# Optimization experiments

Measured on AMD Instinct MI355X. Metric: run time of the kernel, lower is better.

Reference implementation:

```python
import jax, jax.numpy as jnp
import numpy as np

N = 100000       # nodes
E = 1600000      # edges (before self-loops)
D = 128          # input feature dim
H = 128          # hidden width (both hidden GATConv layers)
OUT = 128        # out_channel
NEG_SLOPE = 0.2  # PyG GATConv default


def setup_inputs() -> dict:
    key = jax.random.key(0)
    ks = jax.random.split(key, 16)
    x = jax.random.normal(ks[0], (N, D), dtype=jnp.float32)
    edge_index = jax.random.randint(ks[1], (2, E), 0, N, dtype=jnp.int64)

    def layer_params(k, din, dout):
        k1, k2, k3 = jax.random.split(k, 3)
        W = jax.random.normal(k1, (din, dout), dtype=jnp.float32) * (1.0 / np.sqrt(din))
        a_src = jax.random.normal(k2, (dout,), dtype=jnp.float32) * 0.1
        a_dst = jax.random.normal(k3, (dout,), dtype=jnp.float32) * 0.1
        b = jnp.zeros((dout,), dtype=jnp.float32)
        return W, a_src, a_dst, b

    W0, as0, ad0, b0 = layer_params(ks[2], D, H)
    W1, as1, ad1, b1 = layer_params(ks[3], H, H)
    W2, as2, ad2, b2 = layer_params(ks[4], H, OUT)
    return {
        "x": x, "edge_index": edge_index,
        "W0": W0, "as0": as0, "ad0": ad0, "b0": b0,
        "W1": W1, "as1": as1, "ad1": ad1, "b1": b1,
        "W2": W2, "as2": as2, "ad2": ad2, "b2": b2,
    }


def _gat_conv(x, src, dst, W, a_src, a_dst, b):
    """PyG GATConv, heads=1: gather -> edge attention softmax (per dst) -> scatter-add."""
    h = x @ W                                  # [N, C]
    alpha_s = h @ a_src                        # [N] per-source scalar
    alpha_d = h @ a_dst                        # [N] per-dest scalar
    e = jax.nn.leaky_relu(alpha_s[src] + alpha_d[dst], NEG_SLOPE)  # [Etot]
    # numerically stable softmax over edges grouped by destination node
    m = jax.ops.segment_max(e, dst, num_segments=N)
    ex = jnp.exp(e - m[dst])
    denom = jax.ops.segment_sum(ex, dst, num_segments=N)
    w = ex / denom[dst]                        # [Etot] attention coeffs
    out = jax.ops.segment_sum(h[src] * w[:, None], dst, num_segments=N)
    return out + b


def reference(x, edge_index, W0, as0, ad0, b0, W1, as1, ad1, b1, W2, as2, ad2, b2):
    # GATConv adds self-loops by default; edge_index[0]=source j, [1]=target i
    loops = jnp.arange(N, dtype=edge_index.dtype)
    src = jnp.concatenate([edge_index[0], loops])
    dst = jnp.concatenate([edge_index[1], loops])

    h = jax.nn.relu(_gat_conv(x, src, dst, W0, as0, ad0, b0))
    h = jax.nn.relu(_gat_conv(h, src, dst, W1, as1, ad1, b1))
    return _gat_conv(h, src, dst, W2, as2, ad2, b2)
```

## Files before the change

kernel.cpp:

```cpp
#include <hip/hip_runtime.h>

#define NN 100000
#define EE 1600000
#define NB 391
#define CHUNK 2048

typedef __attribute__((ext_vector_type(8))) short bf16x8;
typedef __attribute__((ext_vector_type(4))) float f32x4;

union BV8 { bf16x8 v; uint4 u; };

static __device__ __forceinline__ unsigned short f2bf(float f) {
  unsigned u = __float_as_uint(f);
  u += 0x7fffu + ((u >> 16) & 1u);
  return (unsigned short)(u >> 16);
}
static __device__ __forceinline__ float bf2f(unsigned short s) {
  return __uint_as_float(((unsigned)s) << 16);
}
static __device__ __forceinline__ unsigned cvt_pk_bf16(float a, float b) {
  unsigned r;
  asm("v_cvt_pk_bf16_f32 %0, %1, %2" : "=v"(r) : "v"(a), "v"(b));
  return r;
}
static __device__ __forceinline__ float bflo(unsigned u) { return __uint_as_float(u << 16); }
static __device__ __forceinline__ float bfhi(unsigned u) { return __uint_as_float(u & 0xffff0000u); }


__global__ void zero_aux(int* __restrict__ bcnt, int* __restrict__ bfill) {
  int i = blockIdx.x * 256 + threadIdx.x;
  if (i < NB * 16) { bcnt[i] = 0; bfill[i] = 0; }
}

__launch_bounds__(256)
__global__ void bucket_hist(const int* __restrict__ dst, int* __restrict__ bcnt) {
  __shared__ int hist[NB];
  int tid = threadIdx.x;
  for (int i = tid; i < NB; i += 256) hist[i] = 0;
  __syncthreads();
  int e0 = blockIdx.x * CHUNK;
  int n = min(CHUNK, EE - e0);
  for (int i = tid; i < n; i += 256) atomicAdd(&hist[dst[e0 + i] >> 8], 1);
  __syncthreads();
  for (int i = tid; i < NB; i += 256) {
    int c = hist[i];
    if (c) atomicAdd(&bcnt[i * 16], c);
  }
}

__launch_bounds__(256)
__global__ void bucket_scan(const int* __restrict__ bcnt, int* __restrict__ bOffC,
                            int* __restrict__ offsets) {
  __shared__ int wpart[4];
  __shared__ int carryS;
  int tid = threadIdx.x, lane = tid & 63, w = tid >> 6;
  if (tid == 0) carryS = 0;
  __syncthreads();
  for (int base = 0; base < NB; base += 256) {
    int i = base + tid;
    int v = (i < NB) ? bcnt[i * 16] : 0;
    int x = v;
    #pragma unroll
    for (int d = 1; d < 64; d <<= 1) { int y = __shfl_up(x, d); if (lane >= d) x += y; }
    if (lane == 63) wpart[w] = x;
    __syncthreads();
    int wbase = 0;
    #pragma unroll
    for (int k = 0; k < 3; ++k) if (k < w) wbase += wpart[k];
    int tot = wpart[0] + wpart[1] + wpart[2] + wpart[3];
    int carry = carryS;
    if (i < NB) bOffC[i] = carry + wbase + x - v;
    __syncthreads();
    if (tid == 0) carryS = carry + tot;
    __syncthreads();
  }
  if (tid == 0) offsets[NN] = EE + NN;
}

__launch_bounds__(256)
__global__ void bucket_scatter(const int* __restrict__ ei, const int* __restrict__ bOffC,
                               int* __restrict__ bfill, long long* __restrict__ pairs) {
  __shared__ int hist[NB];
  __shared__ int lofs[NB];
  __shared__ int resv[NB];
  __shared__ long long stage[CHUNK];
  __shared__ int wpart[4];
  int tid = threadIdx.x, lane = tid & 63, w = tid >> 6;
  int e0 = blockIdx.x * CHUNK;
  int n = min(CHUNK, EE - e0);
  for (int i = tid; i < NB; i += 256) hist[i] = 0;
  __syncthreads();

  int s[8], d[8], lp[8], bk[8];
  #pragma unroll
  for (int q = 0; q < 8; ++q) {
    int i = q * 256 + tid;
    if (i < n) {
      s[q] = ei[e0 + i];
      d[q] = ei[EE + e0 + i];
      bk[q] = d[q] >> 8;
      lp[q] = atomicAdd(&hist[bk[q]], 1);
    }
  }
  __syncthreads();

  int carry = 0;
  for (int base = 0; base < NB; base += 256) {
    int i = base + tid;
    int v = (i < NB) ? hist[i] : 0;
    int x = v;
    #pragma unroll
    for (int dd = 1; dd < 64; dd <<= 1) { int y = __shfl_up(x, dd); if (lane >= dd) x += y; }
    if (lane == 63) wpart[w] = x;
    __syncthreads();
    int wbase = 0;
    #pragma unroll
    for (int k = 0; k < 3; ++k) if (k < w) wbase += wpart[k];
    int tot = wpart[0] + wpart[1] + wpart[2] + wpart[3];
    if (i < NB) lofs[i] = carry + wbase + x - v;
    __syncthreads();
    carry += tot;
  }

  #pragma unroll
  for (int q = 0; q < 8; ++q) {
    int i = q * 256 + tid;
    if (i < n) stage[lofs[bk[q]] + lp[q]] = ((long long)d[q] << 32) | (unsigned)s[q];
  }
  for (int b = tid; b < NB; b += 256) {
    int c = hist[b];
    resv[b] = c ? atomicAdd(&bfill[b * 16], c) : 0;
  }
  __syncthreads();
  for (int i = tid; i < n; i += 256) {
    long long pd = stage[i];
    int dd = (int)(pd >> 32);
    int b = dd >> 8;
    pairs[(size_t)bOffC[b] + resv[b] + (i - lofs[b])] = pd;
  }
}

__launch_bounds__(256)
__global__ void build_csr(const long long* __restrict__ pairs, const int* __restrict__ bOffC,
                          const int* __restrict__ bcnt, int* __restrict__ offsets,
                          int* __restrict__ srcs) {
  __shared__ int deg[256];
  __shared__ int intra[256];
  __shared__ int fil[256];
  __shared__ int wpart[4];
  int b = blockIdx.x, tid = threadIdx.x;
  int n0 = b << 8;
  int nodes = min(256, NN - n0);
  int ecnt = bcnt[b * 16];
  size_t pbase = (size_t)bOffC[b];
  int cbase = bOffC[b] + n0;
  deg[tid] = 0; fil[tid] = 0;
  __syncthreads();
  for (int i = tid; i < ecnt; i += 256) {
    int dd = (int)(pairs[pbase + i] >> 32);
    atomicAdd(&deg[dd - n0], 1);
  }
  __syncthreads();
  int v = (tid < nodes) ? deg[tid] + 1 : 0;
  int lane = tid & 63, w = tid >> 6;
  int x = v;
  #pragma unroll
  for (int dd = 1; dd < 64; dd <<= 1) { int y = __shfl_up(x, dd); if (lane >= dd) x += y; }
  if (lane == 63) wpart[w] = x;
  __syncthreads();
  int wbase = 0;
  #pragma unroll
  for (int k = 0; k < 3; ++k) if (k < w) wbase += wpart[k];
  int excl = wbase + x - v;
  if (tid < nodes) { intra[tid] = excl; offsets[n0 + tid] = cbase + excl; }
  __syncthreads();
  for (int i = tid; i < ecnt; i += 256) {
    long long pd = pairs[pbase + i];
    int dd = (int)(pd >> 32), ss = (int)pd;
    int ln = dd - n0;
    int p = atomicAdd(&fil[ln], 1);
    srcs[cbase + intra[ln] + p] = ss;
  }
  __syncthreads();
  if (tid < nodes) srcs[cbase + intra[tid] + deg[tid]] = n0 + tid;
}


__global__ void prep_w3(const float* __restrict__ Wa, const float* __restrict__ Wb,
                        const float* __restrict__ Wc, short* __restrict__ Whi,
                        short* __restrict__ Wlo) {
  int t = blockIdx.x * 256 + threadIdx.x;
  int L = t >> 11;
  int tt = t & 2047;
  const float* W = (L == 0) ? Wa : (L == 1) ? Wb : Wc;
  int lane = tt & 63, ct = (tt >> 6) & 7, kt = tt >> 9;
  int l4 = lane & 15, grp = lane >> 4;
  int c = ct * 16 + l4;
  int k0 = kt * 32 + grp * 8;
  bf16x8 hi, lo;
  #pragma unroll
  for (int i = 0; i < 8; ++i) {
    float w = W[(k0 + i) * 128 + c];
    unsigned short h = f2bf(w);
    hi[i] = (short)h;
    lo[i] = (short)f2bf(w - bf2f(h));
  }
  size_t off = (size_t)L * 131072 + ((size_t)(kt * 8 + ct) * 64 + lane) * 8;
  *(bf16x8*)&Whi[off] = hi;
  *(bf16x8*)&Wlo[off] = lo;
}


__launch_bounds__(256)
__global__ void transform_mfma(const float* __restrict__ x,
                               const short* __restrict__ Whi, const short* __restrict__ Wlo,
                               const float* __restrict__ a_src, const float* __restrict__ a_dst,
                               unsigned short* __restrict__ hb,
                               float* __restrict__ alphaS, float* __restrict__ alphaD) {
  __shared__ short WhiS[4096];
  __shared__ short WloS[4096];
  int tid = threadIdx.x;
  int lane = tid & 63, wid = tid >> 6;
  int l4 = lane & 15, grp = lane >> 4;
  int rbase = blockIdx.x * 128 + wid * 32;

  const float* xr[2];
  #pragma unroll
  for (int rt = 0; rt < 2; ++rt) {
    int R = rbase + rt * 16 + l4;
    xr[rt] = x + (size_t)(R < NN ? R : 0) * 128;
  }

  f32x4 acc[2][8];
  #pragma unroll
  for (int rt = 0; rt < 2; ++rt)
    #pragma unroll
    for (int ct = 0; ct < 8; ++ct) acc[rt][ct] = (f32x4)(0.f);

  for (int kt = 0; kt < 4; ++kt) {
    bf16x8 Ahi[2], Alo[2];
    #pragma unroll
    for (int rt = 0; rt < 2; ++rt) {
      const float* p = xr[rt] + kt * 32 + grp * 8;
      float4 v0 = *(const float4*)p;
      float4 v1 = *(const float4*)(p + 4);
      BV8 hi, lo;
      hi.u.x = cvt_pk_bf16(v0.x, v0.y);
      hi.u.y = cvt_pk_bf16(v0.z, v0.w);
      hi.u.z = cvt_pk_bf16(v1.x, v1.y);
      hi.u.w = cvt_pk_bf16(v1.z, v1.w);
      lo.u.x = cvt_pk_bf16(v0.x - bflo(hi.u.x), v0.y - bfhi(hi.u.x));
      lo.u.y = cvt_pk_bf16(v0.z - bflo(hi.u.y), v0.w - bfhi(hi.u.y));
      lo.u.z = cvt_pk_bf16(v1.x - bflo(hi.u.z), v1.y - bfhi(hi.u.z));
      lo.u.w = cvt_pk_bf16(v1.z - bflo(hi.u.w), v1.w - bfhi(hi.u.w));
      Ahi[rt] = hi.v;
      Alo[rt] = lo.v;
    }
    __syncthreads();
    {
      int base = kt * 4096 + tid * 16;
      *(bf16x8*)&WhiS[tid * 16]     = *(const bf16x8*)&Whi[base];
      *(bf16x8*)&WhiS[tid * 16 + 8] = *(const bf16x8*)&Whi[base + 8];
      *(bf16x8*)&WloS[tid * 16]     = *(const bf16x8*)&Wlo[base];
      *(bf16x8*)&WloS[tid * 16 + 8] = *(const bf16x8*)&Wlo[base + 8];
    }
    __syncthreads();
    #pragma unroll
    for (int ct = 0; ct < 8; ++ct) {
      bf16x8 bh = *(const bf16x8*)&WhiS[(ct * 64 + lane) * 8];
      bf16x8 bl = *(const bf16x8*)&WloS[(ct * 64 + lane) * 8];
      #pragma unroll
      for (int rt = 0; rt < 2; ++rt) {
        acc[rt][ct] = __builtin_amdgcn_mfma_f32_16x16x32_bf16(Ahi[rt], bh, acc[rt][ct], 0, 0, 0);
        acc[rt][ct] = __builtin_amdgcn_mfma_f32_16x16x32_bf16(Ahi[rt], bl, acc[rt][ct], 0, 0, 0);
        acc[rt][ct] = __builtin_amdgcn_mfma_f32_16x16x32_bf16(Alo[rt], bh, acc[rt][ct], 0, 0, 0);
      }
    }
  }

  float asv[8], adv[8];
  #pragma unroll
  for (int ct = 0; ct < 8; ++ct) { asv[ct] = a_src[ct * 16 + l4]; adv[ct] = a_dst[ct * 16 + l4]; }

  #pragma unroll
  for (int rt = 0; rt < 2; ++rt) {
    #pragma unroll
    for (int reg = 0; reg < 4; ++reg) {
      float ps = 0.f, pd = 0.f;
      #pragma unroll
      for (int ct = 0; ct < 8; ++ct) {
        ps = fmaf(acc[rt][ct][reg], asv[ct], ps);
        pd = fmaf(acc[rt][ct][reg], adv[ct], pd);
      }
      #pragma unroll
      for (int mdl = 1; mdl < 16; mdl <<= 1) {
        ps += __shfl_xor(ps, mdl);
        pd += __shfl_xor(pd, mdl);
      }
      int row = rbase + rt * 16 + grp * 4 + reg;
      if (l4 == 0 && row < NN) { alphaS[row] = ps; alphaD[row] = pd; }
    }
    #pragma unroll
    for (int reg = 0; reg < 4; ++reg) {
      int row = rbase + rt * 16 + grp * 4 + reg;
      if (row < NN) {
        #pragma unroll
        for (int ct = 0; ct < 8; ct += 2) {
          unsigned u = cvt_pk_bf16(acc[rt][ct][reg], acc[rt][ct + 1][reg]);
          hb[(size_t)row * 128 + ct * 16 + l4]       = (unsigned short)u;
          hb[(size_t)row * 128 + (ct + 1) * 16 + l4] = (unsigned short)(u >> 16);
        }
      }
    }
  }
}


template<bool RELU>
__launch_bounds__(256)
__global__ void agg_kernel(const unsigned short* __restrict__ hb,
                           const float* __restrict__ alphaS, const float* __restrict__ alphaD,
                           const int* __restrict__ offsets, const int* __restrict__ srcs,
                           const float* __restrict__ bias, float* __restrict__ out) {
  int lane = threadIdx.x & 63;
  int node = (blockIdx.x * 256 + threadIdx.x) >> 6;
  if (node >= NN) return;
  int beg = offsets[node], end = offsets[node + 1];
  float aD = alphaD[node];

  int l4 = lane & 15, grp = lane >> 4;
  float a[8];
  #pragma unroll
  for (int i = 0; i < 8; ++i) a[i] = 0.f;
  float ssum = 0.f;

  for (int j0 = beg; j0 < end; j0 += 64) {
    int j = j0 + lane;
    int cnt = min(64, end - j0);
    int s = 0; float t = 0.f;
    if (j < end) {
      int sv = srcs[j];
      float e = alphaS[sv] + aD;
      e = (e >= 0.f) ? e : 0.2f * e;
      t = __expf(e);
      s = sv;
    }
    ssum += t;
    for (int jj = 0; jj < cnt; jj += 16) {
      int eA = jj + grp;
      int eB = eA + 4, eC = eA + 8, eD = eA + 12;
      int svA = __shfl(s, eA); float tA = __shfl(t, eA);
      int svB = __shfl(s, eB); float tB = __shfl(t, eB);
      int svC = __shfl(s, eC); float tC = __shfl(t, eC);
      int svD = __shfl(s, eD); float tD = __shfl(t, eD);
      if (tA > 0.f) {
        uint4 h0 = *(const uint4*)&hb[(size_t)svA * 128 + l4 * 8];
        uint4 h1 = *(const uint4*)&hb[(size_t)svB * 128 + l4 * 8];
        a[0] = fmaf(tA, __uint_as_float(h0.x << 16),         a[0]);
        a[1] = fmaf(tA, __uint_as_float(h0.x & 0xffff0000u), a[1]);
        a[2] = fmaf(tA, __uint_as_float(h0.y << 16),         a[2]);
        a[3] = fmaf(tA, __uint_as_float(h0.y & 0xffff0000u), a[3]);
        a[4] = fmaf(tA, __uint_as_float(h0.z << 16),         a[4]);
        a[5] = fmaf(tA, __uint_as_float(h0.z & 0xffff0000u), a[5]);
        a[6] = fmaf(tA, __uint_as_float(h0.w << 16),         a[6]);
        a[7] = fmaf(tA, __uint_as_float(h0.w & 0xffff0000u), a[7]);
        a[0] = fmaf(tB, __uint_as_float(h1.x << 16),         a[0]);
        a[1] = fmaf(tB, __uint_as_float(h1.x & 0xffff0000u), a[1]);
        a[2] = fmaf(tB, __uint_as_float(h1.y << 16),         a[2]);
        a[3] = fmaf(tB, __uint_as_float(h1.y & 0xffff0000u), a[3]);
        a[4] = fmaf(tB, __uint_as_float(h1.z << 16),         a[4]);
        a[5] = fmaf(tB, __uint_as_float(h1.z & 0xffff0000u), a[5]);
        a[6] = fmaf(tB, __uint_as_float(h1.w << 16),         a[6]);
        a[7] = fmaf(tB, __uint_as_float(h1.w & 0xffff0000u), a[7]);
      }
      if (tC > 0.f) {
        uint4 h2 = *(const uint4*)&hb[(size_t)svC * 128 + l4 * 8];
        uint4 h3 = *(const uint4*)&hb[(size_t)svD * 128 + l4 * 8];
        a[0] = fmaf(tC, __uint_as_float(h2.x << 16),         a[0]);
        a[1] = fmaf(tC, __uint_as_float(h2.x & 0xffff0000u), a[1]);
        a[2] = fmaf(tC, __uint_as_float(h2.y << 16),         a[2]);
        a[3] = fmaf(tC, __uint_as_float(h2.y & 0xffff0000u), a[3]);
        a[4] = fmaf(tC, __uint_as_float(h2.z << 16),         a[4]);
        a[5] = fmaf(tC, __uint_as_float(h2.z & 0xffff0000u), a[5]);
        a[6] = fmaf(tC, __uint_as_float(h2.w << 16),         a[6]);
        a[7] = fmaf(tC, __uint_as_float(h2.w & 0xffff0000u), a[7]);
        a[0] = fmaf(tD, __uint_as_float(h3.x << 16),         a[0]);
        a[1] = fmaf(tD, __uint_as_float(h3.x & 0xffff0000u), a[1]);
        a[2] = fmaf(tD, __uint_as_float(h3.y << 16),         a[2]);
        a[3] = fmaf(tD, __uint_as_float(h3.y & 0xffff0000u), a[3]);
        a[4] = fmaf(tD, __uint_as_float(h3.z << 16),         a[4]);
        a[5] = fmaf(tD, __uint_as_float(h3.z & 0xffff0000u), a[5]);
        a[6] = fmaf(tD, __uint_as_float(h3.w << 16),         a[6]);
        a[7] = fmaf(tD, __uint_as_float(h3.w & 0xffff0000u), a[7]);
      }
    }
  }
  #pragma unroll
  for (int d2 = 1; d2 < 64; d2 <<= 1) ssum += __shfl_xor(ssum, d2);
  float inv = 1.f / ssum;

  #pragma unroll
  for (int i = 0; i < 8; ++i) {
    a[i] += __shfl_xor(a[i], 16);
    a[i] += __shfl_xor(a[i], 32);
  }
  if (grp == 0) {
    float4 b0 = *(const float4*)&bias[l4 * 8];
    float4 b1 = *(const float4*)&bias[l4 * 8 + 4];
    float4 o0 = {fmaf(a[0], inv, b0.x), fmaf(a[1], inv, b0.y),
                 fmaf(a[2], inv, b0.z), fmaf(a[3], inv, b0.w)};
    float4 o1 = {fmaf(a[4], inv, b1.x), fmaf(a[5], inv, b1.y),
                 fmaf(a[6], inv, b1.z), fmaf(a[7], inv, b1.w)};
    if (RELU) {
      o0.x = fmaxf(o0.x, 0.f); o0.y = fmaxf(o0.y, 0.f);
      o0.z = fmaxf(o0.z, 0.f); o0.w = fmaxf(o0.w, 0.f);
      o1.x = fmaxf(o1.x, 0.f); o1.y = fmaxf(o1.y, 0.f);
      o1.z = fmaxf(o1.z, 0.f); o1.w = fmaxf(o1.w, 0.f);
    }
    *(float4*)&out[(size_t)node * 128 + l4 * 8]     = o0;
    *(float4*)&out[(size_t)node * 128 + l4 * 8 + 4] = o1;
  }
}


extern "C" void kernel_launch(void* const* d_in, const int* in_sizes, int n_in,
                              void* d_out, int out_size, void* d_ws, size_t ws_size,
                              hipStream_t stream) {
  const float* x   = (const float*)d_in[0];
  const int*   ei  = (const int*)d_in[1];
  const float* W0  = (const float*)d_in[2];
  const float* as0 = (const float*)d_in[3];
  const float* ad0 = (const float*)d_in[4];
  const float* b0  = (const float*)d_in[5];
  const float* W1  = (const float*)d_in[6];
  const float* as1 = (const float*)d_in[7];
  const float* ad1 = (const float*)d_in[8];
  const float* b1  = (const float*)d_in[9];
  const float* W2  = (const float*)d_in[10];
  const float* as2 = (const float*)d_in[11];
  const float* ad2 = (const float*)d_in[12];
  const float* b2  = (const float*)d_in[13];
  float* out = (float*)d_out;

  long long* pairs = (long long*)d_ws;
  short* Whi = (short*)(pairs + EE);
  short* Wlo = Whi + 3 * 131072;
  unsigned short* hb = (unsigned short*)(Wlo + 3 * 131072);
  float* alphaS = (float*)(hb + (size_t)NN * 128);
  float* alphaD = alphaS + NN;
  int*   offsets = (int*)(alphaD + NN);
  int*   srcs    = offsets + NN + 1;
  int*   bcnt    = srcs + EE + NN;
  int*   bfill   = bcnt + NB * 16;
  int*   bOffC   = bfill + NB * 16;

  const int cgrid = (EE + CHUNK - 1) / CHUNK;

  prep_w3<<<24, 256, 0, stream>>>(W0, W1, W2, Whi, Wlo);
  zero_aux<<<(NB * 16 + 255) / 256, 256, 0, stream>>>(bcnt, bfill);
  bucket_hist<<<cgrid, 256, 0, stream>>>(ei + EE, bcnt);
  bucket_scan<<<1, 256, 0, stream>>>(bcnt, bOffC, offsets);
  bucket_scatter<<<cgrid, 256, 0, stream>>>(ei, bOffC, bfill, pairs);
  build_csr<<<NB, 256, 0, stream>>>(pairs, bOffC, bcnt, offsets, srcs);

  const int tgrid = (NN + 127) / 128;
  const int agrid = (NN + 3) / 4;

  transform_mfma<<<tgrid, 256, 0, stream>>>(x, Whi, Wlo, as0, ad0, hb, alphaS, alphaD);
  agg_kernel<true><<<agrid, 256, 0, stream>>>(hb, alphaS, alphaD, offsets, srcs, b0, out);

  transform_mfma<<<tgrid, 256, 0, stream>>>(out, Whi + 131072, Wlo + 131072, as1, ad1, hb, alphaS, alphaD);
  agg_kernel<true><<<agrid, 256, 0, stream>>>(hb, alphaS, alphaD, offsets, srcs, b1, out);

  transform_mfma<<<tgrid, 256, 0, stream>>>(out, Whi + 262144, Wlo + 262144, as2, ad2, hb, alphaS, alphaD);
  agg_kernel<false><<<agrid, 256, 0, stream>>>(hb, alphaS, alphaD, offsets, srcs, b2, out);
}
```

Baseline: 358.3 us.

## Fold attention vectors into GEMM tile and pack CSR pairs to 32 bits

Precomputes W·a_src and W·a_dst per layer and appends them as a ninth MFMA column tile, so alpha scores come straight out of the matrix multiply instead of per-row FMA and shuffle reductions. It also packs edge pairs as an 8-bit local destination plus a 24-bit source, which halves the bytes written by bucket_scatter and read by build_csr. In exchange, each transform does about 12% more MFMA work, and the alpha values are computed in a different rounding order.

```diff
diff --git a/kernel.cpp b/kernel.cpp
--- a/kernel.cpp
+++ b/kernel.cpp
@@ -4,6 +4,7 @@
 #define EE 1600000
 #define NB 391
 #define CHUNK 2048
+#define LFRAG 18432
 
 typedef __attribute__((ext_vector_type(8))) short bf16x8;
 typedef __attribute__((ext_vector_type(4))) float f32x4;
@@ -79,11 +80,12 @@
 
 __launch_bounds__(256)
 __global__ void bucket_scatter(const int* __restrict__ ei, const int* __restrict__ bOffC,
-                               int* __restrict__ bfill, long long* __restrict__ pairs) {
+                               int* __restrict__ bfill, unsigned* __restrict__ pairs) {
   __shared__ int hist[NB];
   __shared__ int lofs[NB];
   __shared__ int resv[NB];
-  __shared__ long long stage[CHUNK];
+  __shared__ unsigned stage[CHUNK];
+  __shared__ unsigned short stageB[CHUNK];
   __shared__ int wpart[4];
   int tid = threadIdx.x, lane = tid & 63, w = tid >> 6;
   int e0 = blockIdx.x * CHUNK;
@@ -125,7 +127,11 @@
   #pragma unroll
   for (int q = 0; q < 8; ++q) {
     int i = q * 256 + tid;
-    if (i < n) stage[lofs[bk[q]] + lp[q]] = ((long long)d[q] << 32) | (unsigned)s[q];
+    if (i < n) {
+      int p = lofs[bk[q]] + lp[q];
+      stage[p]  = ((unsigned)(d[q] & 255) << 24) | (unsigned)s[q];
+      stageB[p] = (unsigned short)bk[q];
+    }
   }
   for (int b = tid; b < NB; b += 256) {
     int c = hist[b];
@@ -133,15 +139,13 @@
   }
   __syncthreads();
   for (int i = tid; i < n; i += 256) {
-    long long pd = stage[i];
-    int dd = (int)(pd >> 32);
-    int b = dd >> 8;
-    pairs[(size_t)bOffC[b] + resv[b] + (i - lofs[b])] = pd;
-  }
-}
-
-__launch_bounds__(256)
-__global__ void build_csr(const long long* __restrict__ pairs, const int* __restrict__ bOffC,
+    int b = stageB[i];
+    pairs[(size_t)bOffC[b] + resv[b] + (i - lofs[b])] = stage[i];
+  }
+}
+
+__launch_bounds__(256)
+__global__ void build_csr(const unsigned* __restrict__ pairs, const int* __restrict__ bOffC,
                           const int* __restrict__ bcnt, int* __restrict__ offsets,
                           int* __restrict__ srcs) {
   __shared__ int deg[256];
@@ -157,8 +161,8 @@
   deg[tid] = 0; fil[tid] = 0;
   __syncthreads();
   for (int i = tid; i < ecnt; i += 256) {
-    int dd = (int)(pairs[pbase + i] >> 32);
-    atomicAdd(&deg[dd - n0], 1);
+    int ln = (int)(pairs[pbase + i] >> 24);
+    atomicAdd(&deg[ln], 1);
   }
   __syncthreads();
   int v = (tid < nodes) ? deg[tid] + 1 : 0;
@@ -175,9 +179,8 @@
   if (tid < nodes) { intra[tid] = excl; offsets[n0 + tid] = cbase + excl; }
   __syncthreads();
   for (int i = tid; i < ecnt; i += 256) {
-    long long pd = pairs[pbase + i];
-    int dd = (int)(pd >> 32), ss = (int)pd;
-    int ln = dd - n0;
+    unsigned pd = pairs[pbase + i];
+    int ln = (int)(pd >> 24), ss = (int)(pd & 0xFFFFFFu);
     int p = atomicAdd(&fil[ln], 1);
     srcs[cbase + intra[ln] + p] = ss;
   }
@@ -186,26 +189,56 @@
 }
 
 
+__global__ void prep_wavec(const float* __restrict__ Wa, const float* __restrict__ Wb,
+                           const float* __restrict__ Wc,
+                           const float* __restrict__ s0, const float* __restrict__ d0,
+                           const float* __restrict__ s1, const float* __restrict__ d1,
+                           const float* __restrict__ s2, const float* __restrict__ d2,
+                           float* __restrict__ was, float* __restrict__ wad) {
+  int t = blockIdx.x * 256 + threadIdx.x;
+  if (t >= 384) return;
+  int L = t >> 7, k = t & 127;
+  const float* W  = (L == 0) ? Wa : (L == 1) ? Wb : Wc;
+  const float* as = (L == 0) ? s0 : (L == 1) ? s1 : s2;
+  const float* ad = (L == 0) ? d0 : (L == 1) ? d1 : d2;
+  float accs = 0.f, accd = 0.f;
+  for (int c = 0; c < 128; c += 4) {
+    float4 w = *(const float4*)&W[k * 128 + c];
+    float4 a = *(const float4*)&as[c];
+    float4 b = *(const float4*)&ad[c];
+    accs += w.x * a.x + w.y * a.y + w.z * a.z + w.w * a.w;
+    accd += w.x * b.x + w.y * b.y + w.z * b.z + w.w * b.w;
+  }
+  was[t] = accs;
+  wad[t] = accd;
+}
+
 __global__ void prep_w3(const float* __restrict__ Wa, const float* __restrict__ Wb,
-                        const float* __restrict__ Wc, short* __restrict__ Whi,
+                        const float* __restrict__ Wc, const float* __restrict__ was,
+                        const float* __restrict__ wad, short* __restrict__ Whi,
                         short* __restrict__ Wlo) {
   int t = blockIdx.x * 256 + threadIdx.x;
-  int L = t >> 11;
-  int tt = t & 2047;
+  if (t >= 6912) return;
+  int L = t / 2304, tt = t % 2304;
+  int kt = tt / 576, rem = tt % 576;
+  int ct = rem >> 6, lane = rem & 63;
   const float* W = (L == 0) ? Wa : (L == 1) ? Wb : Wc;
-  int lane = tt & 63, ct = (tt >> 6) & 7, kt = tt >> 9;
   int l4 = lane & 15, grp = lane >> 4;
-  int c = ct * 16 + l4;
   int k0 = kt * 32 + grp * 8;
   bf16x8 hi, lo;
   #pragma unroll
   for (int i = 0; i < 8; ++i) {
-    float w = W[(k0 + i) * 128 + c];
+    float w;
+    if (ct < 8) {
+      w = W[(k0 + i) * 128 + ct * 16 + l4];
+    } else {
+      w = (l4 == 0) ? was[L * 128 + k0 + i] : (l4 == 1) ? wad[L * 128 + k0 + i] : 0.f;
+    }
     unsigned short h = f2bf(w);
     hi[i] = (short)h;
     lo[i] = (short)f2bf(w - bf2f(h));
   }
-  size_t off = (size_t)L * 131072 + ((size_t)(kt * 8 + ct) * 64 + lane) * 8;
+  size_t off = (size_t)L * LFRAG + ((size_t)(kt * 9 + ct) * 64 + lane) * 8;
   *(bf16x8*)&Whi[off] = hi;
   *(bf16x8*)&Wlo[off] = lo;
 }
@@ -214,11 +247,10 @@
 __launch_bounds__(256)
 __global__ void transform_mfma(const float* __restrict__ x,
                                const short* __restrict__ Whi, const short* __restrict__ Wlo,
-                               const float* __restrict__ a_src, const float* __restrict__ a_dst,
                                unsigned short* __restrict__ hb,
                                float* __restrict__ alphaS, float* __restrict__ alphaD) {
-  __shared__ short WhiS[4096];
-  __shared__ short WloS[4096];
+  __shared__ short WhiS[4608];
+  __shared__ short WloS[4608];
   int tid = threadIdx.x;
   int lane = tid & 63, wid = tid >> 6;
   int l4 = lane & 15, grp = lane >> 4;
@@ -231,11 +263,11 @@
     xr[rt] = x + (size_t)(R < NN ? R : 0) * 128;
   }
 
-  f32x4 acc[2][8];
+  f32x4 acc[2][9];
   #pragma unroll
   for (int rt = 0; rt < 2; ++rt)
     #pragma unroll
-    for (int ct = 0; ct < 8; ++ct) acc[rt][ct] = (f32x4)(0.f);
+    for (int ct = 0; ct < 9; ++ct) acc[rt][ct] = (f32x4)(0.f);
 
   for (int kt = 0; kt < 4; ++kt) {
     bf16x8 Ahi[2], Alo[2];
@@ -258,15 +290,15 @@
     }
     __syncthreads();
     {
-      int base = kt * 4096 + tid * 16;
-      *(bf16x8*)&WhiS[tid * 16]     = *(const bf16x8*)&Whi[base];
-      *(bf16x8*)&WhiS[tid * 16 + 8] = *(const bf16x8*)&Whi[base + 8];
-      *(bf16x8*)&WloS[tid * 16]     = *(const bf16x8*)&Wlo[base];
-      *(bf16x8*)&WloS[tid * 16 + 8] = *(const bf16x8*)&Wlo[base + 8];
-    }
-    __syncthreads();
-    #pragma unroll
-    for (int ct = 0; ct < 8; ++ct) {
+      const bf16x8* gh = (const bf16x8*)Whi + kt * 576;
+      const bf16x8* gl = (const bf16x8*)Wlo + kt * 576;
+      bf16x8* sh = (bf16x8*)WhiS;
+      bf16x8* sl = (bf16x8*)WloS;
+      for (int i = tid; i < 576; i += 256) { sh[i] = gh[i]; sl[i] = gl[i]; }
+    }
+    __syncthreads();
+    #pragma unroll
+    for (int ct = 0; ct < 9; ++ct) {
       bf16x8 bh = *(const bf16x8*)&WhiS[(ct * 64 + lane) * 8];
       bf16x8 bl = *(const bf16x8*)&WloS[(ct * 64 + lane) * 8];
       #pragma unroll
@@ -278,32 +310,14 @@
     }
   }
 
-  float asv[8], adv[8];
-  #pragma unroll
-  for (int ct = 0; ct < 8; ++ct) { asv[ct] = a_src[ct * 16 + l4]; adv[ct] = a_dst[ct * 16 + l4]; }
-
   #pragma unroll
   for (int rt = 0; rt < 2; ++rt) {
-    #pragma unroll
-    for (int reg = 0; reg < 4; ++reg) {
-      float ps = 0.f, pd = 0.f;
-      #pragma unroll
-      for (int ct = 0; ct < 8; ++ct) {
-        ps = fmaf(acc[rt][ct][reg], asv[ct], ps);
-        pd = fmaf(acc[rt][ct][reg], adv[ct], pd);
-      }
-      #pragma unroll
-      for (int mdl = 1; mdl < 16; mdl <<= 1) {
-        ps += __shfl_xor(ps, mdl);
-        pd += __shfl_xor(pd, mdl);
-      }
-      int row = rbase + rt * 16 + grp * 4 + reg;
-      if (l4 == 0 && row < NN) { alphaS[row] = ps; alphaD[row] = pd; }
-    }
     #pragma unroll
     for (int reg = 0; reg < 4; ++reg) {
       int row = rbase + rt * 16 + grp * 4 + reg;
       if (row < NN) {
+        if (l4 == 0)      alphaS[row] = acc[rt][8][reg];
+        else if (l4 == 1) alphaD[row] = acc[rt][8][reg];
         #pragma unroll
         for (int ct = 0; ct < 8; ct += 2) {
           unsigned u = cvt_pk_bf16(acc[rt][ct][reg], acc[rt][ct + 1][reg]);
@@ -442,10 +456,12 @@
   const float* b2  = (const float*)d_in[13];
   float* out = (float*)d_out;
 
-  long long* pairs = (long long*)d_ws;
-  short* Whi = (short*)(pairs + EE);
-  short* Wlo = Whi + 3 * 131072;
-  unsigned short* hb = (unsigned short*)(Wlo + 3 * 131072);
+  float*    was   = (float*)d_ws;
+  float*    wad   = was + 384;
+  unsigned* pairs = (unsigned*)(wad + 384);
+  short*    Whi   = (short*)(pairs + EE);
+  short*    Wlo   = Whi + 3 * LFRAG;
+  unsigned short* hb = (unsigned short*)(Wlo + 3 * LFRAG);
   float* alphaS = (float*)(hb + (size_t)NN * 128);
   float* alphaD = alphaS + NN;
   int*   offsets = (int*)(alphaD + NN);
@@ -456,7 +472,8 @@
 
   const int cgrid = (EE + CHUNK - 1) / CHUNK;
 
-  prep_w3<<<24, 256, 0, stream>>>(W0, W1, W2, Whi, Wlo);
+  prep_wavec<<<2, 256, 0, stream>>>(W0, W1, W2, as0, ad0, as1, ad1, as2, ad2, was, wad);
+  prep_w3<<<27, 256, 0, stream>>>(W0, W1, W2, was, wad, Whi, Wlo);
   zero_aux<<<(NB * 16 + 255) / 256, 256, 0, stream>>>(bcnt, bfill);
   bucket_hist<<<cgrid, 256, 0, stream>>>(ei + EE, bcnt);
   bucket_scan<<<1, 256, 0, stream>>>(bcnt, bOffC, offsets);
@@ -466,12 +483,12 @@
   const int tgrid = (NN + 127) / 128;
   const int agrid = (NN + 3) / 4;
 
-  transform_mfma<<<tgrid, 256, 0, stream>>>(x, Whi, Wlo, as0, ad0, hb, alphaS, alphaD);
+  transform_mfma<<<tgrid, 256, 0, stream>>>(x, Whi, Wlo, hb, alphaS, alphaD);
   agg_kernel<true><<<agrid, 256, 0, stream>>>(hb, alphaS, alphaD, offsets, srcs, b0, out);
 
-  transform_mfma<<<tgrid, 256, 0, stream>>>(out, Whi + 131072, Wlo + 131072, as1, ad1, hb, alphaS, alphaD);
+  transform_mfma<<<tgrid, 256, 0, stream>>>(out, Whi + LFRAG, Wlo + LFRAG, hb, alphaS, alphaD);
   agg_kernel<true><<<agrid, 256, 0, stream>>>(hb, alphaS, alphaD, offsets, srcs, b1, out);
 
-  transform_mfma<<<tgrid, 256, 0, stream>>>(out, Whi + 262144, Wlo + 262144, as2, ad2, hb, alphaS, alphaD);
+  transform_mfma<<<tgrid, 256, 0, stream>>>(out, Whi + 2 * LFRAG, Wlo + 2 * LFRAG, hb, alphaS, alphaD);
   agg_kernel<false><<<agrid, 256, 0, stream>>>(hb, alphaS, alphaD, offsets, srcs, b2, out);
 }
```

New measurement: 372.0 us. 3.8% more time.
